# Optimization experiments

Hardware: AMD Instinct MI355X
Metric: run time of the kernel (lower is better)

The kernel has to match this reference:

```python
import jax, jax.numpy as jnp
import numpy as np

B, T, D = 4, 2048, 1024
RANK, FACTOR, SUB = 8, 64, 4
S = 4 * SUB  # 16


def construct_hamilton(A):
    # A: [rank, 4, sub, sub] -> [rank, 4*sub, 4*sub]
    r, i, j, k = A[:, 0], A[:, 1], A[:, 2], A[:, 3]
    return jnp.concatenate([
        jnp.concatenate([r, -i, -j, -k], axis=2),
        jnp.concatenate([i, r, -k, j], axis=2),
        jnp.concatenate([j, k, r, -i], axis=2),
        jnp.concatenate([k, -j, i, r], axis=2),
    ], axis=1)


def setup_inputs() -> dict:
    key = jax.random.key(0)
    k1, k2, k3 = jax.random.split(key, 3)
    x = jax.random.normal(k1, (B, T, D), dtype=jnp.float32)
    A = jax.random.normal(k2, (RANK, 4, SUB, SUB), dtype=jnp.float32)
    # orthogonal-ish init with (r+1)^-0.5 scaling, like the torch init
    fB = jax.random.normal(k3, (RANK, FACTOR, FACTOR), dtype=jnp.float32)
    q, _ = jnp.linalg.qr(fB)
    scale = (jnp.arange(RANK, dtype=jnp.float32) + 1.0) ** -0.5
    factors_B = q * scale[:, None, None]
    bias = jnp.zeros((D,), dtype=jnp.float32)
    return {"x": x, "A": A, "factors_B": factors_B, "bias": bias}


def reference(x, A, factors_B, bias):
    Bb, Tt, Dd = x.shape
    x_flat = x.reshape(-1, S, FACTOR)          # [N, s, i]
    H = construct_hamilton(A)                   # [r, k, s]
    wav = jnp.einsum('nsi,rji->rnsj', x_flat, factors_B)  # [r, N, s, j]
    out = jnp.einsum('rnsj,rks->nkj', wav, H)   # [N, k, j]
    return out.reshape(Bb, Tt, Dd) + bias
```

## Files before the change

kernel.cpp:

```cpp
#include <hip/hip_runtime.h>
#include <stdint.h>

#define RANKS 8
#define MDIM 8192
#define KDIM 1024
#define NDIM 1024
#define BM 128
#define BN 128
#define BK 32
#define NT (KDIM / BK)
#define THREADS 256

typedef __bf16 bf16x8 __attribute__((ext_vector_type(8)));
typedef float f32x4 __attribute__((ext_vector_type(4)));

__device__ __forceinline__ unsigned short f2bf(float f) {
  union { float f; uint32_t u; } v; v.f = f;
  uint32_t u = v.u;
  u += 0x7FFFu + ((u >> 16) & 1u);
  return (unsigned short)(u >> 16);
}

__constant__ int   c_comp[4][4] = {{0,1,2,3},{1,0,3,2},{2,3,0,1},{3,2,1,0}};
__constant__ float c_sign[4][4] = {{1.f,-1.f,-1.f,-1.f},
                                   {1.f, 1.f,-1.f, 1.f},
                                   {1.f, 1.f, 1.f,-1.f},
                                   {1.f,-1.f, 1.f, 1.f}};

__global__ void build_W(const float* __restrict__ A, const float* __restrict__ fB,
                        unsigned short* __restrict__ W) {
  int idx = blockIdx.x * 256 + threadIdx.x;
  int p  = idx >> 8;
  int q4 = (idx & 255) << 2;
  int k = p >> 6, j = p & 63;
  int kb = k >> 2, ks = k & 3;
  int s = q4 >> 6;
  int sb = s >> 2, ss = s & 3;
  int   comp = c_comp[kb][sb];
  float sgn  = c_sign[kb][sb];
  float o0 = 0.f, o1 = 0.f, o2 = 0.f, o3 = 0.f;
  int i0 = q4 & 63;
#pragma unroll
  for (int r = 0; r < RANKS; ++r) {
    float h = sgn * A[r * 64 + comp * 16 + ks * 4 + ss];
    const float* fb = fB + r * 4096 + j * 64 + i0;
    o0 += h * fb[0]; o1 += h * fb[1]; o2 += h * fb[2]; o3 += h * fb[3];
  }
  ushort4 st;
  st.x = f2bf(o0); st.y = f2bf(o1); st.z = f2bf(o2); st.w = f2bf(o3);
  *reinterpret_cast<ushort4*>(W + (size_t)p * KDIM + q4) = st;
}

__device__ __forceinline__ void gload16(const void* g, void* l) {
  __builtin_amdgcn_global_load_lds(
      (const __attribute__((address_space(1))) unsigned int*)(uintptr_t)g,
      (__attribute__((address_space(3))) unsigned int*)(uintptr_t)l,
      16, 0, 0);
}

__global__ __launch_bounds__(THREADS, 3) void gemm_ham(
    const float* __restrict__ x, const unsigned short* __restrict__ W,
    const float* __restrict__ bias, float* __restrict__ out) {
  __shared__ float          Asm_[2][BM * BK];
  __shared__ unsigned short Bsm_[2][BN * BK];

  const int tid  = threadIdx.x;
  const int lane = tid & 63;
  const int wid  = tid >> 6;
  const int wr   = wid >> 1;
  const int wc   = wid & 1;
  const int rb   = lane & 15;
  const int qtr  = lane >> 4;

  const int flat = blockIdx.x;
  const int xg = flat & 7, ig = flat >> 3;
  const int bx = xg * 8 + (ig >> 3);
  const int by = ig & 7;
  const int row0 = bx * BM;
  const int col0 = by * BN;

  f32x4 acc[4][4];
  f32x4 zero = {0.f, 0.f, 0.f, 0.f};
#pragma unroll
  for (int m = 0; m < 4; ++m)
#pragma unroll
    for (int n = 0; n < 4; ++n) acc[m][n] = zero;

  auto stageA = [&](int kt, int slot) {
#pragma unroll
    for (int g = 0; g < 4; ++g) {
      int id = g * 256 + tid;
      int r = id >> 3, ct = id & 7;
      gload16(x + (size_t)(row0 + r) * KDIM + kt * BK + ((ct ^ (r & 7)) << 2),
              &Asm_[slot][id * 4]);
    }
  };
  auto stageB = [&](int kt, int slot) {
#pragma unroll
    for (int g = 0; g < 2; ++g) {
      int id = g * 256 + tid;
      int r = id >> 2, ct = id & 3;
      gload16(W + (size_t)(col0 + r) * KDIM + kt * BK + ((ct ^ ((r >> 1) & 3)) << 3),
              &Bsm_[slot][id * 8]);
    }
  };

  stageA(0, 0); stageB(0, 0);
  __syncthreads();

  int cur = 0;
#pragma unroll 1
  for (int t = 0; t < NT; ++t) {
    if (t + 1 < NT) { stageA(t + 1, cur ^ 1); stageB(t + 1, cur ^ 1); }

    const char* Ab = reinterpret_cast<const char*>(&Asm_[cur][0]);
    const char* Bb = reinterpret_cast<const char*>(&Bsm_[cur][0]);
    bf16x8 af[4], bfr[4];
#pragma unroll
    for (int m = 0; m < 4; ++m) {
      int r = wr * 64 + m * 16 + rb;
      int u0 = (qtr * 2)     ^ (r & 7);
      int u1 = (qtr * 2 + 1) ^ (r & 7);
      f32x4 lo = *reinterpret_cast<const f32x4*>(Ab + r * 128 + (u0 << 4));
      f32x4 hi = *reinterpret_cast<const f32x4*>(Ab + r * 128 + (u1 << 4));
      bf16x8 v;
      v[0] = (__bf16)lo[0]; v[1] = (__bf16)lo[1]; v[2] = (__bf16)lo[2]; v[3] = (__bf16)lo[3];
      v[4] = (__bf16)hi[0]; v[5] = (__bf16)hi[1]; v[6] = (__bf16)hi[2]; v[7] = (__bf16)hi[3];
      af[m] = v;
    }
#pragma unroll
    for (int n = 0; n < 4; ++n) {
      int r = wc * 64 + n * 16 + rb;
      int u = qtr ^ ((r >> 1) & 3);
      bfr[n] = *reinterpret_cast<const bf16x8*>(Bb + r * 64 + (u << 4));
    }

#pragma unroll
    for (int m = 0; m < 4; ++m)
#pragma unroll
      for (int n = 0; n < 4; ++n)
        acc[m][n] = __builtin_amdgcn_mfma_f32_16x16x32_bf16(af[m], bfr[n], acc[m][n], 0, 0, 0);

    __syncthreads();
    cur ^= 1;
  }

  const int crow = row0 + wr * 64 + qtr * 4;
  const int ccol = col0 + wc * 64 + rb;
#pragma unroll
  for (int n = 0; n < 4; ++n) {
    int c = ccol + n * 16;
    float bv = bias[c];
#pragma unroll
    for (int m = 0; m < 4; ++m)
#pragma unroll
      for (int v = 0; v < 4; ++v)
        out[(size_t)(crow + m * 16 + v) * NDIM + c] = acc[m][n][v] + bv;
  }
}

__global__ void fallback_kernel(const float* __restrict__ x, const float* __restrict__ A,
                                const float* __restrict__ fB, const float* __restrict__ bias,
                                float* __restrict__ out) {
  __shared__ float xrow[1024];
  const int n = blockIdx.x;
  const int tid = threadIdx.x;
  for (int t = tid; t < 1024; t += 256) xrow[t] = x[(size_t)n * 1024 + t];
  __syncthreads();
  for (int pp = 0; pp < 4; ++pp) {
    int p = pp * 256 + tid;
    int k = p >> 6, j = p & 63;
    int kb = k >> 2, ks = k & 3;
    float accv = 0.f;
    for (int s = 0; s < 16; ++s) {
      int sb = s >> 2, ss = s & 3;
      int comp = c_comp[kb][sb];
      float sgn = c_sign[kb][sb];
      float hA[RANKS];
#pragma unroll
      for (int r = 0; r < RANKS; ++r) hA[r] = sgn * A[r * 64 + comp * 16 + ks * 4 + ss];
      for (int i = 0; i < 64; ++i) {
        float w = 0.f;
#pragma unroll
        for (int r = 0; r < RANKS; ++r) w += hA[r] * fB[r * 4096 + j * 64 + i];
        accv += xrow[s * 64 + i] * w;
      }
    }
    out[(size_t)n * 1024 + p] = accv + bias[p];
  }
}

extern "C" void kernel_launch(void* const* d_in, const int* in_sizes, int n_in,
                              void* d_out, int out_size, void* d_ws, size_t ws_size,
                              hipStream_t stream) {
  const float* x    = (const float*)d_in[0];
  const float* A    = (const float*)d_in[1];
  const float* fB   = (const float*)d_in[2];
  const float* bias = (const float*)d_in[3];
  float* out = (float*)d_out;

  const size_t needW = (size_t)NDIM * KDIM * sizeof(unsigned short);
  if (ws_size >= needW) {
    unsigned short* W = (unsigned short*)d_ws;
    build_W<<<dim3(1024), dim3(256), 0, stream>>>(A, fB, W);
    gemm_ham<<<dim3((MDIM / BM) * (NDIM / BN)), dim3(THREADS), 0, stream>>>(x, W, bias, out);
  } else {
    fallback_kernel<<<dim3(MDIM), dim3(256), 0, stream>>>(x, A, fB, bias, out);
  }
}
```

Before: 38.17 us.

## Shrink N tile to 64 and read W fragments directly from global

Halves the block N tile, which doubles the grid to 1024 blocks. Each of the four waves now owns 32 rows across all 64 columns. The B operand (bf16 W) is no longer staged through LDS; each wave loads its MFMA fragments straight from global/L2 every k-step, and occupancy is raised to 4 blocks. The aim is to cut LDS footprint and the B staging work to gain occupancy and parallelism. In exchange, the uncoalesced B loads are exposed on the critical path without double buffering, and the fp32 x tile is reloaded twice as often overall.

After: 86.24 us. +125.9%, slower.

```diff
diff --git a/kernel.cpp b/kernel.cpp
--- a/kernel.cpp
+++ b/kernel.cpp
@@ -6,7 +6,7 @@
 #define KDIM 1024
 #define NDIM 1024
 #define BM 128
-#define BN 128
+#define BN 64
 #define BK 32
 #define NT (KDIM / BK)
 #define THREADS 256
@@ -58,31 +58,28 @@
       16, 0, 0);
 }
 
-__global__ __launch_bounds__(THREADS, 3) void gemm_ham(
+__global__ __launch_bounds__(THREADS, 4) void gemm_ham(
     const float* __restrict__ x, const unsigned short* __restrict__ W,
     const float* __restrict__ bias, float* __restrict__ out) {
-  __shared__ float          Asm_[2][BM * BK];
-  __shared__ unsigned short Bsm_[2][BN * BK];
+  __shared__ float Asm_[2][BM * BK];
 
   const int tid  = threadIdx.x;
   const int lane = tid & 63;
   const int wid  = tid >> 6;
-  const int wr   = wid >> 1;
-  const int wc   = wid & 1;
   const int rb   = lane & 15;
   const int qtr  = lane >> 4;
 
   const int flat = blockIdx.x;
   const int xg = flat & 7, ig = flat >> 3;
-  const int bx = xg * 8 + (ig >> 3);
-  const int by = ig & 7;
+  const int bx = xg * 8 + (ig >> 4);
+  const int by = ig & 15;
   const int row0 = bx * BM;
   const int col0 = by * BN;
 
-  f32x4 acc[4][4];
+  f32x4 acc[2][4];
   f32x4 zero = {0.f, 0.f, 0.f, 0.f};
 #pragma unroll
-  for (int m = 0; m < 4; ++m)
+  for (int m = 0; m < 2; ++m)
 #pragma unroll
     for (int n = 0; n < 4; ++n) acc[m][n] = zero;
 
@@ -95,30 +92,26 @@
               &Asm_[slot][id * 4]);
     }
   };
-  auto stageB = [&](int kt, int slot) {
-#pragma unroll
-    for (int g = 0; g < 2; ++g) {
-      int id = g * 256 + tid;
-      int r = id >> 2, ct = id & 3;
-      gload16(W + (size_t)(col0 + r) * KDIM + kt * BK + ((ct ^ ((r >> 1) & 3)) << 3),
-              &Bsm_[slot][id * 8]);
-    }
-  };
 
-  stageA(0, 0); stageB(0, 0);
+  stageA(0, 0);
   __syncthreads();
 
   int cur = 0;
 #pragma unroll 1
   for (int t = 0; t < NT; ++t) {
-    if (t + 1 < NT) { stageA(t + 1, cur ^ 1); stageB(t + 1, cur ^ 1); }
+    if (t + 1 < NT) stageA(t + 1, cur ^ 1);
+
+    bf16x8 bfr[4];
+#pragma unroll
+    for (int n = 0; n < 4; ++n)
+      bfr[n] = *reinterpret_cast<const bf16x8*>(
+          W + (size_t)(col0 + n * 16 + rb) * KDIM + t * BK + qtr * 8);
 
     const char* Ab = reinterpret_cast<const char*>(&Asm_[cur][0]);
-    const char* Bb = reinterpret_cast<const char*>(&Bsm_[cur][0]);
-    bf16x8 af[4], bfr[4];
+    bf16x8 af[2];
 #pragma unroll
-    for (int m = 0; m < 4; ++m) {
-      int r = wr * 64 + m * 16 + rb;
+    for (int m = 0; m < 2; ++m) {
+      int r = wid * 32 + m * 16 + rb;
       int u0 = (qtr * 2)     ^ (r & 7);
       int u1 = (qtr * 2 + 1) ^ (r & 7);
       f32x4 lo = *reinterpret_cast<const f32x4*>(Ab + r * 128 + (u0 << 4));
@@ -128,15 +121,9 @@
       v[4] = (__bf16)hi[0]; v[5] = (__bf16)hi[1]; v[6] = (__bf16)hi[2]; v[7] = (__bf16)hi[3];
       af[m] = v;
     }
-#pragma unroll
-    for (int n = 0; n < 4; ++n) {
-      int r = wc * 64 + n * 16 + rb;
-      int u = qtr ^ ((r >> 1) & 3);
-      bfr[n] = *reinterpret_cast<const bf16x8*>(Bb + r * 64 + (u << 4));
-    }
 
 #pragma unroll
-    for (int m = 0; m < 4; ++m)
+    for (int m = 0; m < 2; ++m)
 #pragma unroll
       for (int n = 0; n < 4; ++n)
         acc[m][n] = __builtin_amdgcn_mfma_f32_16x16x32_bf16(af[m], bfr[n], acc[m][n], 0, 0, 0);
@@ -145,14 +132,14 @@
     cur ^= 1;
   }
 
-  const int crow = row0 + wr * 64 + qtr * 4;
-  const int ccol = col0 + wc * 64 + rb;
+  const int crow = row0 + wid * 32 + qtr * 4;
+  const int ccol = col0 + rb;
 #pragma unroll
   for (int n = 0; n < 4; ++n) {
     int c = ccol + n * 16;
     float bv = bias[c];
 #pragma unroll
-    for (int m = 0; m < 4; ++m)
+    for (int m = 0; m < 2; ++m)
 #pragma unroll
       for (int v = 0; v < 4; ++v)
         out[(size_t)(crow + m * 16 + v) * NDIM + c] = acc[m][n][v] + bv;
```
